# Optimization experiments

Hardware: AMD Instinct MI355X
Metric: run time of the kernel (lower is better)

The kernel has to match this reference:

```python
import jax, jax.numpy as jnp
import numpy as np

C = 1203      # num_classes
P = 0.8       # mitigation exponent
Q = 2.0       # compensation exponent
EPS = 0.01
LOSS_WEIGHT = 1.0


def setup_inputs() -> dict:
    key = jax.random.key(0)
    k1, k2 = jax.random.split(key)
    N = 32768
    cls_score = jax.random.normal(k1, (N, C + 2), dtype=jnp.float32)
    labels = jax.random.randint(k2, (N,), 0, C, dtype=jnp.int64)  # all positive RoIs
    label_weights = jnp.ones((N,), dtype=jnp.float32)
    return {
        'cls_score': cls_score,
        'labels': labels,
        'label_weights': label_weights,
        'avg_factor': N,
    }


def _seesaw_loss(cls_score, labels, label_weights, avg_factor):
    N = cls_score.shape[0]
    rows = jnp.arange(N)

    # cum_samples buffer: starts at zero, incremented by per-class counts this step
    cum = jnp.zeros((C + 1,), cls_score.dtype).at[labels].add(1.0)

    # one-hot multi-labels over C+1 channels (last channel is background, unused since all labels < C)
    m_labels = jax.nn.one_hot(labels, C + 1, dtype=cls_score.dtype)  # [N, C+1]

    csc = cls_score[:, :C]   # class logits [N, C]
    csb = cls_score[:, C:]   # binary (pos/neg) logits [N, 2]

    # --- seesaw weights ---
    cum_c = jnp.maximum(cum, 1.0)
    ratio = cum_c[None, :] / cum_c[:, None]                 # [C+1, C+1]
    sample_w = jnp.where(ratio < 1.0, ratio ** P, 1.0)
    mitigation = sample_w[labels]                           # [N, C+1]

    scores = jax.lax.stop_gradient(jax.nn.softmax(csc, axis=1))  # detached
    self_scores = scores[rows, labels]                      # [N]
    score_mat = scores / jnp.maximum(self_scores, EPS)[:, None]  # [N, C]
    compensation = jnp.where(score_mat > 1.0, score_mat ** Q, 1.0)

    seesaw = mitigation.at[:, :C].multiply(compensation)    # [N, C+1]

    # add log seesaw weights to negative-class logits
    adj = csc + (jnp.log(seesaw) * (1.0 - m_labels))[:, :C]  # [N, C]

    # --- multi-label cross entropy (per-row masked logsumexp + softplus) ---
    lw = label_weights[:, None]
    pos_mask = m_labels[:, :C] * lw            # [N, C]
    neg_mask = (1.0 - m_labels[:, :C]) * lw
    ninf = jnp.array(-jnp.inf, adj.dtype)
    pos_lse = jax.nn.logsumexp(jnp.where(pos_mask == 1.0, -adj, ninf), axis=1)
    neg_lse = jax.nn.logsumexp(jnp.where(neg_mask == 1.0, adj, ninf), axis=1)
    inv_pos_log = -jnp.log(pos_mask.sum(axis=1))
    loss_classes = LOSS_WEIGHT * jax.nn.softplus(inv_pos_log + pos_lse + neg_lse).sum() / avg_factor

    # --- binary objectness cross entropy ---
    b_labels = (labels == C).astype(jnp.int32)  # all zero here
    ce = -jax.nn.log_softmax(csb, axis=1)[rows, b_labels]
    loss_binary = (ce * label_weights).sum() / avg_factor

    return loss_classes + loss_binary


def reference(cls_score, labels, label_weights, avg_factor):
    return _seesaw_loss(cls_score, labels, label_weights, avg_factor)
```

## Files before the change

### kernel.cpp

```cpp
#include <hip/hip_runtime.h>


#define C_CLS   1203
#define ROW_LEN 1205
#define NBINS   1204
#define RPAD    1280
#define NEG_HUGE (-3.402823466e38f)
#define LOG2E    1.4426950408889634f
#define LN2      0.6931471805599453f
#define LOG_EPS2 (-6.643856189774724f)
#define P_POW    0.8f
#define Q_POW    2.0f
#define M2FIX    16.0f

#if __has_builtin(__builtin_amdgcn_exp2f)
#define EXP2(x) __builtin_amdgcn_exp2f(x)
#else
#define EXP2(x) exp2f(x)
#endif
#if __has_builtin(__builtin_amdgcn_logf)
#define LOG2F_(x) __builtin_amdgcn_logf(x)
#else
#define LOG2F_(x) __log2f(x)
#endif

__launch_bounds__(1024)
__global__ void prep_k(const int* __restrict__ labels, int N,
                       float* __restrict__ plgG) {
    __shared__ unsigned hist[NBINS];
    for (int i = threadIdx.x; i < NBINS; i += 1024) hist[i] = 0u;
    __syncthreads();

    const int nv = N >> 2;
    const int4* lp = (const int4*)labels;
    for (int i = threadIdx.x; i < nv; i += 1024) {
        int4 v = lp[i];
        atomicAdd(&hist[v.x], 1u); atomicAdd(&hist[v.y], 1u);
        atomicAdd(&hist[v.z], 1u); atomicAdd(&hist[v.w], 1u);
    }
    for (int i = (N & ~3) + (int)threadIdx.x; i < N; i += 1024)
        atomicAdd(&hist[labels[i]], 1u);
    __syncthreads();

    for (int u = threadIdx.x; u < RPAD; u += 1024) {
        #pragma unroll
        for (int kk = 0; kk < 4; ++kk) {
            int j = u + kk;
            float v = 0.0f;
            if (j < NBINS) v = P_POW * LOG2F_(fmaxf((float)hist[j], 1.0f));
            plgG[kk * RPAD + u] = v;
        }
    }
}

__launch_bounds__(256)
__global__ void seesaw_row_k(const float* __restrict__ cls,
                             const int* __restrict__ labels,
                             const float* __restrict__ lweights,
                             const float* __restrict__ plgG,
                             float* __restrict__ wsums,
                             int N) {
    __shared__ __align__(16) float plg[4][RPAD];
    {
        const float4* src = (const float4*)plgG;
        float4* dst = (float4*)&plg[0][0];
        for (int i = threadIdx.x; i < RPAD; i += 256) dst[i] = src[i];
    }
    __syncthreads();

    const int lane = threadIdx.x & 63;
    const int wv   = threadIdx.x >> 6;
    const int wid  = blockIdx.x * 4 + wv;
    const int nw   = gridDim.x * 4;

    float acc = 0.0f;
    int n = wid;
    if (n < N) {
        const int k = (-n) & 3;
        int   labc = labels[n];
        float wc   = lweights[n];

        for (;;) {
            const int  n2    = n + nw;
            const bool have2 = (n2 < N);
            int labn = 0; float wn = 0.0f;
            if (have2) { labn = labels[n2]; wn = lweights[n2]; }

            const float* row = cls + (size_t)n * ROW_LEN;
            const float labv = row[labc];
            const float c0   = row[C_CLS];
            const float c1   = row[C_CLS + 1];

            const float4* vp = (const float4*)(row + k);
            float4 q[5];
            #pragma unroll
            for (int i = 0; i < 4; ++i) q[i] = vp[(size_t)i * 64 + lane];
            {
                int b4 = k + 1024 + 4 * lane;
                float4 t = make_float4(NEG_HUGE, NEG_HUGE, NEG_HUGE, NEG_HUGE);
                if (b4 + 3 <= C_CLS - 1) {
                    t = vp[(size_t)256 + lane];
                } else {
                    if (b4     <= C_CLS - 1) t.x = row[b4];
                    if (b4 + 1 <= C_CLS - 1) t.y = row[b4 + 1];
                    if (b4 + 2 <= C_CLS - 1) t.z = row[b4 + 2];
                }
                q[4] = t;
            }
            float pv = (lane < k) ? row[lane] : NEG_HUGE;

            pv *= LOG2E;
            float s = EXP2(pv - M2FIX);
            #pragma unroll
            for (int i = 0; i < 5; ++i) {
                q[i].x *= LOG2E; q[i].y *= LOG2E;
                q[i].z *= LOG2E; q[i].w *= LOG2E;
                s += EXP2(q[i].x - M2FIX) + EXP2(q[i].y - M2FIX)
                   + EXP2(q[i].z - M2FIX) + EXP2(q[i].w - M2FIX);
            }
            #pragma unroll
            for (int o = 32; o > 0; o >>= 1) s += __shfl_xor(s, o, 64);

            const float L2    = M2FIX + LOG2F_(s);
            const float labv2 = labv * LOG2E;
            const float G     = fmaxf(labv2, L2 + LOG_EPS2);
            const float W     = L2 + Q_POW * (L2 - G);
            const float plogl = plg[0][labc];
            const float Wp    = W + plogl;
            const float mW    = -W;

            float T;
            {
                float t = fminf(plg[0][lane] - Wp, mW);
                float h = fmaxf(pv - G, 0.0f);
                T = EXP2(fmaf(Q_POW, h, pv) + t);
            }
            #pragma unroll
            for (int i = 0; i < 5; ++i) {
                const float4 lg = *(const float4*)&plg[k][256 * i + 4 * lane];
                { float t = fminf(lg.x - Wp, mW), h = fmaxf(q[i].x - G, 0.f);
                  T += EXP2(fmaf(Q_POW, h, q[i].x) + t); }
                { float t = fminf(lg.y - Wp, mW), h = fmaxf(q[i].y - G, 0.f);
                  T += EXP2(fmaf(Q_POW, h, q[i].y) + t); }
                { float t = fminf(lg.z - Wp, mW), h = fmaxf(q[i].z - G, 0.f);
                  T += EXP2(fmaf(Q_POW, h, q[i].z) + t); }
                { float t = fminf(lg.w - Wp, mW), h = fmaxf(q[i].w - G, 0.f);
                  T += EXP2(fmaf(Q_POW, h, q[i].w) + t); }
            }
            #pragma unroll
            for (int o = 32; o > 0; o >>= 1) T += __shfl_xor(T, o, 64);
            T -= EXP2(labv2 - W);
            T = fmaxf(T, 1e-37f);

            const float nl2 = W + LOG2F_(T);
            const float xx  = (nl2 - labv2) * LN2;
            const float rl  = (xx > 0.0f) ? (xx + log1pf(__expf(-xx)))
                                          : log1pf(__expf(xx));
            const float mm   = fmaxf(c0, c1);
            const float lseb = mm + __logf(__expf(c0 - mm) + __expf(c1 - mm));
            const float ce   = lseb - ((labc == C_CLS) ? c1 : c0);
            const float rlw  = (wc == 1.0f) ? rl : 0.0f;
            acc += rlw + ce * wc;

            if (!have2) break;
            n = n2; labc = labn; wc = wn;
        }
    }

    if (lane == 0) wsums[wid] = acc;
}

__launch_bounds__(512)
__global__ void reduce_k(const float* __restrict__ wsums, int nb,
                         const int* __restrict__ avg_raw,
                         float* __restrict__ out) {
    int tid = threadIdx.x;
    float s = 0.0f;
    int nb4 = nb >> 2;
    const float4* bp = (const float4*)wsums;
    for (int i = tid; i < nb4; i += 512) {
        float4 v = bp[i];
        s += (v.x + v.y) + (v.z + v.w);
    }
    for (int i = (nb4 << 2) + tid; i < nb; i += 512) s += wsums[i];

    #pragma unroll
    for (int o = 32; o > 0; o >>= 1) s += __shfl_xor(s, o, 64);

    __shared__ float ws8[8];
    int lane = tid & 63, wvi = tid >> 6;
    if (lane == 0) ws8[wvi] = s;
    __syncthreads();
    if (tid == 0) {
        float t = 0.0f;
        #pragma unroll
        for (int i = 0; i < 8; ++i) t += ws8[i];
        int ai = avg_raw[0];
        float af;
        if (ai > 0 && ai < (1 << 26)) {
            af = (float)ai;
        } else {
            union { int i; float f; } u;
            u.i = ai;
            af = u.f;
        }
        out[0] = t / af;
    }
}

extern "C" void kernel_launch(void* const* d_in, const int* in_sizes, int n_in,
                              void* d_out, int out_size, void* d_ws, size_t ws_size,
                              hipStream_t stream) {
    const float* cls    = (const float*)d_in[0];
    const int*   labels = (const int*)d_in[1];
    const float* lw     = (const float*)d_in[2];
    const int*   avgp   = (const int*)d_in[3];
    float*       out    = (float*)d_out;

    const int N = in_sizes[1];

    float* plgG  = (float*)d_ws;
    float* wsums = (float*)d_ws + 4 * RPAD;

    int g = (N + 15) / 16;
    if (g > 2048) g = 2048;
    if (g < 1) g = 1;

    prep_k<<<1, 1024, 0, stream>>>(labels, N, plgG);
    seesaw_row_k<<<g, 256, 0, stream>>>(cls, labels, lw, plgG, wsums, N);
    reduce_k<<<1, 512, 0, stream>>>(wsums, g * 4, avgp, out);
}
```

Before: 50.86 us.

## Parallelize label histogram across blocks with global atomics and move log-table build into row kernel

Replaces the single-block prep kernel, which histogrammed all labels in shared memory and wrote a 4-shifted log-count table, with a multi-block histogram kernel that uses global atomics into a zeroed buffer. Each row-kernel block now rebuilds the shifted log2 table in shared memory directly from the counts. This removes a serialized one-block pass over all labels but adds a memset launch, global atomic contention across 1204 bins, and redundant per-block log computation.

```diff
diff --git a/kernel.cpp b/kernel.cpp
--- a/kernel.cpp
+++ b/kernel.cpp
@@ -24,47 +24,37 @@
 #define LOG2F_(x) __log2f(x)
 #endif
 
-__launch_bounds__(1024)
-__global__ void prep_k(const int* __restrict__ labels, int N,
-                       float* __restrict__ plgG) {
-    __shared__ unsigned hist[NBINS];
-    for (int i = threadIdx.x; i < NBINS; i += 1024) hist[i] = 0u;
-    __syncthreads();
-
+__launch_bounds__(256)
+__global__ void hist_k(const int* __restrict__ labels, unsigned* __restrict__ cum, int N) {
+    const int i = blockIdx.x * blockDim.x + threadIdx.x;
     const int nv = N >> 2;
     const int4* lp = (const int4*)labels;
-    for (int i = threadIdx.x; i < nv; i += 1024) {
+    if (i < nv) {
         int4 v = lp[i];
-        atomicAdd(&hist[v.x], 1u); atomicAdd(&hist[v.y], 1u);
-        atomicAdd(&hist[v.z], 1u); atomicAdd(&hist[v.w], 1u);
-    }
-    for (int i = (N & ~3) + (int)threadIdx.x; i < N; i += 1024)
-        atomicAdd(&hist[labels[i]], 1u);
-    __syncthreads();
-
-    for (int u = threadIdx.x; u < RPAD; u += 1024) {
-        #pragma unroll
-        for (int kk = 0; kk < 4; ++kk) {
-            int j = u + kk;
-            float v = 0.0f;
-            if (j < NBINS) v = P_POW * LOG2F_(fmaxf((float)hist[j], 1.0f));
-            plgG[kk * RPAD + u] = v;
-        }
-    }
+        atomicAdd(&cum[v.x], 1u); atomicAdd(&cum[v.y], 1u);
+        atomicAdd(&cum[v.z], 1u); atomicAdd(&cum[v.w], 1u);
+    }
+    if (blockIdx.x == 0 && (int)threadIdx.x < (N & 3))
+        atomicAdd(&cum[labels[(N & ~3) + threadIdx.x]], 1u);
 }
 
 __launch_bounds__(256)
 __global__ void seesaw_row_k(const float* __restrict__ cls,
                              const int* __restrict__ labels,
                              const float* __restrict__ lweights,
-                             const float* __restrict__ plgG,
+                             const unsigned* __restrict__ cum,
                              float* __restrict__ wsums,
                              int N) {
     __shared__ __align__(16) float plg[4][RPAD];
-    {
-        const float4* src = (const float4*)plgG;
-        float4* dst = (float4*)&plg[0][0];
-        for (int i = threadIdx.x; i < RPAD; i += 256) dst[i] = src[i];
+
+    for (int j = threadIdx.x; j < RPAD + 3; j += 256) {
+        float f = 0.0f;
+        if (j < NBINS) f = P_POW * LOG2F_(fmaxf((float)cum[j], 1.0f));
+        #pragma unroll
+        for (int kk = 0; kk < 4; ++kk) {
+            int u = j - kk;
+            if (u >= 0 && u < RPAD) plg[kk][u] = f;
+        }
     }
     __syncthreads();
 
@@ -219,14 +209,17 @@
 
     const int N = in_sizes[1];
 
-    float* plgG  = (float*)d_ws;
-    float* wsums = (float*)d_ws + 4 * RPAD;
+    unsigned* cum   = (unsigned*)d_ws;
+    float*    wsums = (float*)d_ws + RPAD;
 
     int g = (N + 15) / 16;
     if (g > 2048) g = 2048;
     if (g < 1) g = 1;
 
-    prep_k<<<1, 1024, 0, stream>>>(labels, N, plgG);
-    seesaw_row_k<<<g, 256, 0, stream>>>(cls, labels, lw, plgG, wsums, N);
+    hipMemsetAsync(cum, 0, NBINS * sizeof(unsigned), stream);
+    int hb = ((N >> 2) + 255) / 256;
+    if (hb < 1) hb = 1;
+    hist_k<<<hb, 256, 0, stream>>>(labels, cum, N);
+    seesaw_row_k<<<g, 256, 0, stream>>>(cls, labels, lw, cum, wsums, N);
     reduce_k<<<1, 512, 0, stream>>>(wsums, g * 4, avgp, out);
 }
```

After: 60.41 us. 1.19x slower.
